# Performance work log

Hardware: AMD Instinct MI355X
Metric: run time of the kernel (lower is better)

The kernel has to match this reference:

```python
import jax, jax.numpy as jnp
import numpy as np

B, D_IN, D_H, D_BOT, D_EXP, N_CLS = 8192, 1024, 2048, 512, 1024, 10


def _w(key, shape):
    return jax.random.normal(key, shape, dtype=jnp.float32) * 0.02


def setup_inputs() -> dict:
    key = jax.random.key(0)
    ks = jax.random.split(key, 16)
    return {
        "x": jax.random.normal(ks[0], (B, D_IN), dtype=jnp.float32),
        "labels": jax.random.randint(ks[1], (B,), 0, N_CLS, dtype=jnp.int32),
        # encoder: 1024 -> 2048 -> 512 (ReLU after each)
        "W1": _w(ks[2], (D_IN, D_H)), "b1": jnp.zeros((D_H,), jnp.float32),
        "W2": _w(ks[3], (D_H, D_BOT)), "b2": jnp.zeros((D_BOT,), jnp.float32),
        # per-class expert MLPs (identical shapes, stacked): 512 -> 1024 -> 512, ReLU after each
        "EW1": _w(ks[4], (N_CLS, D_BOT, D_EXP)), "Eb1": jnp.zeros((N_CLS, D_EXP), jnp.float32),
        "EW2": _w(ks[5], (N_CLS, D_EXP, D_BOT)), "Eb2": jnp.zeros((N_CLS, D_BOT), jnp.float32),
        # decoder: 512 -> 2048 (ReLU) -> 1024 (no final activation)
        "DW1": _w(ks[6], (D_BOT, D_H)), "Db1": jnp.zeros((D_H,), jnp.float32),
        "DW2": _w(ks[7], (D_H, D_IN)), "Db2": jnp.zeros((D_IN,), jnp.float32),
    }


def reference(x, labels, W1, b1, W2, b2, EW1, Eb1, EW2, Eb2, DW1, Db1, DW2, Db2):
    # encoder
    h = jax.nn.relu(x @ W1 + b1)           # [B, 2048]
    h = jax.nn.relu(h @ W2 + b2)           # [B, 512]
    # class-routed experts: compute all experts densely, then gather by label
    he = jax.nn.relu(jnp.einsum('bi,eio->beo', h, EW1) + Eb1[None])   # [B, E, 1024]
    he = jax.nn.relu(jnp.einsum('beh,eho->beo', he, EW2) + Eb2[None]) # [B, E, 512]
    sel = jnp.take_along_axis(he, labels[:, None, None].astype(jnp.int32), axis=1)[:, 0]  # [B, 512]
    # decoder (activation after first layer only)
    d = jax.nn.relu(sel @ DW1 + Db1)       # [B, 2048]
    out = d @ DW2 + Db2                    # [B, 1024]
    return out
```

## Files before the change

kernel.cpp:

```cpp
#include <hip/hip_runtime.h>
#include <hip/hip_bf16.h>
#include <stdint.h>

typedef __attribute__((ext_vector_type(8))) short bf16x8;
typedef __attribute__((ext_vector_type(4))) float f32x4;

__device__ __forceinline__ unsigned short f2bf(float f) {
  unsigned int u = __float_as_uint(f);
  u += 0x7fff + ((u >> 16) & 1);
  return (unsigned short)(u >> 16);
}

__device__ __forceinline__ void gload16(const void* g, void* l) {
  __builtin_amdgcn_global_load_lds(
      (const __attribute__((address_space(1))) void*)g,
      (__attribute__((address_space(3))) void*)l, 16, 0, 0);
}

#define Bsz   8192
#define D_IN  1024
#define D_H   2048
#define D_BOT 512
#define D_EXP 1024
#define N_CLS 10

__global__ __launch_bounds__(1024) void k_route(const int* __restrict__ lab,
                                                int* __restrict__ counts,
                                                int* __restrict__ starts,
                                                int* __restrict__ perm) {
  __shared__ int scnt[N_CLS], scur[N_CLS];
  const int t = threadIdx.x;
  if (t < N_CLS) scnt[t] = 0;
  __syncthreads();
  int myl[8];
#pragma unroll
  for (int i = 0; i < 8; ++i) {
    myl[i] = lab[t * 8 + i];
    atomicAdd(&scnt[myl[i]], 1);
  }
  __syncthreads();
  if (t == 0) {
    int s = 0;
    for (int e = 0; e < N_CLS; ++e) {
      starts[e] = s; scur[e] = s; counts[e] = scnt[e]; s += scnt[e];
    }
  }
  __syncthreads();
#pragma unroll
  for (int i = 0; i < 8; ++i) {
    int p = atomicAdd(&scur[myl[i]], 1);
    perm[p] = t * 8 + i;
  }
}

__global__ void k_cvt(const float* __restrict__ in, unsigned short* __restrict__ out) {
  int i = (blockIdx.x * blockDim.x + threadIdx.x) * 8;
  const float4* p = (const float4*)(in + i);
  float4 a = p[0], b = p[1];
  uint4 o;
  o.x = (unsigned)f2bf(a.x) | ((unsigned)f2bf(a.y) << 16);
  o.y = (unsigned)f2bf(a.z) | ((unsigned)f2bf(a.w) << 16);
  o.z = (unsigned)f2bf(b.x) | ((unsigned)f2bf(b.y) << 16);
  o.w = (unsigned)f2bf(b.z) | ((unsigned)f2bf(b.w) << 16);
  *(uint4*)(out + i) = o;
}

__global__ void k_transpose_cvt(const float* __restrict__ in, unsigned short* __restrict__ out,
                                int K, int N) {
  __shared__ float tile[32][33];
  size_t eoff = (size_t)blockIdx.z * K * N;
  in  += eoff;
  out += eoff;
  int n0 = blockIdx.x * 32, k0 = blockIdx.y * 32;
  int tx = threadIdx.x, ty = threadIdx.y;
#pragma unroll
  for (int i = 0; i < 4; i++) {
    int k = ty + i * 8;
    tile[k][tx] = in[(size_t)(k0 + k) * N + n0 + tx];
  }
  __syncthreads();
#pragma unroll
  for (int i = 0; i < 4; i++) {
    int n = ty + i * 8;
    out[(size_t)(n0 + n) * K + k0 + tx] = f2bf(tile[tx][n]);
  }
}

template <int BM, int BN, bool RELU, bool BF16OUT>
__global__ __launch_bounds__(512, 2) void k_gemm8(
    const unsigned short* __restrict__ A,
    const unsigned short* __restrict__ WT,
    const float* __restrict__ bias,
    void* __restrict__ Cv,
    int M, int N, int K) {
  constexpr int WROWS = BM / 2;
  constexpr int QR = WROWS / 2;
  constexpr int FMq = QR / 16;
  constexpr int ACH = BM / 64;
  constexpr int BCH = BN / 64;

  const int nby = gridDim.y;
  const int nwg = gridDim.x * nby;
  int orig = blockIdx.x + gridDim.x * blockIdx.y;
  int q = nwg >> 3, r = nwg & 7;
  int xcd = orig & 7, idx = orig >> 3;
  int wg = (xcd < r ? xcd * (q + 1) : r * (q + 1) + (xcd - r) * q) + idx;
  int bx = wg / nby, by = wg % nby;
  const int m0 = bx * BM, n0 = by * BN;

  __shared__ __align__(16) unsigned short As[2][BM * 64];
  __shared__ __align__(16) unsigned short Bs[2][BN * 64];

  const int t = threadIdx.x;
  const int l = t & 63;
  const int w = t >> 6;
  const int wm = w >> 2, wn = w & 3;

  const int rl = t >> 3;
  const int sl16 = (t & 7) ^ (rl & 7);
  const unsigned short* asrc[ACH];
  const unsigned short* bsrc[BCH];
#pragma unroll
  for (int i = 0; i < ACH; ++i)
    asrc[i] = A + (size_t)(m0 + i * 64 + rl) * K + sl16 * 8;
#pragma unroll
  for (int i = 0; i < BCH; ++i)
    bsrc[i] = WT + (size_t)(n0 + i * 64 + rl) * K + sl16 * 8;
  const int dst = t * 8;

  auto STAGE = [&](int kt, int buf) {
#pragma unroll
    for (int i = 0; i < ACH; ++i)
      gload16(asrc[i] + kt * 64, &As[buf][i * 4096 + dst]);
#pragma unroll
    for (int i = 0; i < BCH; ++i)
      gload16(bsrc[i] + kt * 64, &Bs[buf][i * 4096 + dst]);
  };

  f32x4 acc[2][2][FMq][2] = {};
  bf16x8 af[FMq][2];
  bf16x8 bq[2][2][2];

  const int la = l & 15;
  const int ko = l >> 4;
  const int arow0 = wm * WROWS + la;
  const int brow0 = wn * 64 + la;

  const int nt = K / 64;
  STAGE(0, 0);

  for (int kt = 0; kt < nt; ++kt) {
    const int cur = kt & 1;
    const char* Ab = (const char*)As[cur];
    const char* Bb = (const char*)Bs[cur];

    asm volatile("s_waitcnt vmcnt(0)" ::: "memory");
    __builtin_amdgcn_s_barrier();
    if (kt + 1 < nt) STAGE(kt + 1, cur ^ 1);
    __builtin_amdgcn_sched_barrier(0);

#pragma unroll
    for (int fm = 0; fm < FMq; ++fm)
#pragma unroll
      for (int ks = 0; ks < 2; ++ks) {
        int row = arow0 + fm * 16;
        int s = ks * 4 + ko;
        af[fm][ks] = *(const bf16x8*)(Ab + (row << 7) + ((s ^ (row & 7)) << 4));
      }
#pragma unroll
    for (int fn = 0; fn < 2; ++fn)
#pragma unroll
      for (int ks = 0; ks < 2; ++ks) {
        int row = brow0 + fn * 16;
        int s = ks * 4 + ko;
        bq[0][fn][ks] = *(const bf16x8*)(Bb + (row << 7) + ((s ^ (row & 7)) << 4));
      }
    __builtin_amdgcn_s_setprio(1);
#pragma unroll
    for (int fm = 0; fm < FMq; ++fm)
#pragma unroll
      for (int fn = 0; fn < 2; ++fn)
#pragma unroll
        for (int ks = 0; ks < 2; ++ks)
          acc[0][0][fm][fn] = __builtin_amdgcn_mfma_f32_16x16x32_bf16(
              af[fm][ks], bq[0][fn][ks], acc[0][0][fm][fn], 0, 0, 0);
    __builtin_amdgcn_s_setprio(0);
    __builtin_amdgcn_s_barrier();

#pragma unroll
    for (int fn = 0; fn < 2; ++fn)
#pragma unroll
      for (int ks = 0; ks < 2; ++ks) {
        int row = brow0 + 32 + fn * 16;
        int s = ks * 4 + ko;
        bq[1][fn][ks] = *(const bf16x8*)(Bb + (row << 7) + ((s ^ (row & 7)) << 4));
      }
    __builtin_amdgcn_s_setprio(1);
#pragma unroll
    for (int fm = 0; fm < FMq; ++fm)
#pragma unroll
      for (int fn = 0; fn < 2; ++fn)
#pragma unroll
        for (int ks = 0; ks < 2; ++ks)
          acc[0][1][fm][fn] = __builtin_amdgcn_mfma_f32_16x16x32_bf16(
              af[fm][ks], bq[1][fn][ks], acc[0][1][fm][fn], 0, 0, 0);
    __builtin_amdgcn_s_setprio(0);
    __builtin_amdgcn_s_barrier();

#pragma unroll
    for (int fm = 0; fm < FMq; ++fm)
#pragma unroll
      for (int ks = 0; ks < 2; ++ks) {
        int row = arow0 + QR + fm * 16;
        int s = ks * 4 + ko;
        af[fm][ks] = *(const bf16x8*)(Ab + (row << 7) + ((s ^ (row & 7)) << 4));
      }
    __builtin_amdgcn_s_setprio(1);
#pragma unroll
    for (int fm = 0; fm < FMq; ++fm)
#pragma unroll
      for (int fn = 0; fn < 2; ++fn)
#pragma unroll
        for (int ks = 0; ks < 2; ++ks)
          acc[1][0][fm][fn] = __builtin_amdgcn_mfma_f32_16x16x32_bf16(
              af[fm][ks], bq[0][fn][ks], acc[1][0][fm][fn], 0, 0, 0);
    __builtin_amdgcn_s_setprio(0);
    __builtin_amdgcn_s_barrier();

    __builtin_amdgcn_s_setprio(1);
#pragma unroll
    for (int fm = 0; fm < FMq; ++fm)
#pragma unroll
      for (int fn = 0; fn < 2; ++fn)
#pragma unroll
        for (int ks = 0; ks < 2; ++ks)
          acc[1][1][fm][fn] = __builtin_amdgcn_mfma_f32_16x16x32_bf16(
              af[fm][ks], bq[1][fn][ks], acc[1][1][fm][fn], 0, 0, 0);
    __builtin_amdgcn_s_setprio(0);
  }
  asm volatile("s_waitcnt vmcnt(0)" ::: "memory");

  const int crow0 = m0 + wm * WROWS;
  const int ccol0 = n0 + wn * 64;
#pragma unroll
  for (int qn = 0; qn < 2; ++qn)
#pragma unroll
    for (int fn = 0; fn < 2; ++fn) {
      int c = ccol0 + qn * 32 + fn * 16 + la;
      float bv = bias[c];
#pragma unroll
      for (int qm = 0; qm < 2; ++qm)
#pragma unroll
        for (int fm = 0; fm < FMq; ++fm)
#pragma unroll
          for (int j = 0; j < 4; ++j) {
            int rr = crow0 + qm * QR + fm * 16 + (ko << 2) + j;
            float v = acc[qm][qn][fm][fn][j] + bv;
            if (RELU) v = fmaxf(v, 0.0f);
            if (BF16OUT) ((unsigned short*)Cv)[(size_t)rr * N + c] = f2bf(v);
            else         ((float*)Cv)[(size_t)rr * N + c] = v;
          }
    }
}

template <int TBM, int TBN, int WM, int WN,
          bool RELU, bool BF16OUT, bool GROUPED, bool SCATTER, bool GATHER>
__global__ __launch_bounds__(256) void k_gemm(
    const unsigned short* __restrict__ A,
    const unsigned short* __restrict__ WT,
    const float* __restrict__ bias,
    void* __restrict__ Cv,
    int M, int N, int K,
    const int* __restrict__ starts, const int* __restrict__ counts,
    const int* __restrict__ perm) {
  constexpr int FM = TBM / WM / 16;
  constexpr int FN = TBN / WN / 16;
  constexpr int ALOADS = TBM / 64;
  constexpr int BLOADS = TBN / 64;
  constexpr int LDS_LD = ALOADS + BLOADS;

  const int nby = gridDim.y;
  const int nwg = gridDim.x * nby;
  int orig = blockIdx.x + gridDim.x * blockIdx.y;
  int q = nwg >> 3, r = nwg & 7;
  int xcd = orig & 7, idx = orig >> 3;
  int wg = (xcd < r ? xcd * (q + 1) : r * (q + 1) + (xcd - r) * q) + idx;
  int bx = wg / nby, by = wg % nby;

  int Meff, start = 0, mo;
  const unsigned short* Wp = WT;
  const float* biasp = bias;
  if (GROUPED) {
    int bxr = bx;
    int found = 0;
#pragma unroll
    for (int e = 0; e < N_CLS; ++e) {
      int c = counts[e];
      int nb = (c + TBM - 1) / TBM;
      if (!found && bxr < nb) {
        found = 1; Meff = c; start = starts[e]; mo = bxr * TBM;
        Wp = WT + (size_t)e * N * K; biasp = bias + (size_t)e * N;
      }
      if (!found) bxr -= nb;
    }
    if (!found) return;
    if (!GATHER) A += (size_t)start * K;
  } else {
    Meff = M; mo = bx * TBM;
  }
  const int n0 = by * TBN;

  __shared__ __align__(16) unsigned short As[3][TBM * 32];
  __shared__ __align__(16) unsigned short Bs[3][TBN * 32];

  const int t = threadIdx.x;
  const int l = t & 63;
  const int w = t >> 6;
  const int wm = (w / WN) * (TBM / WM);
  const int wn = (w % WN) * (TBN / WN);

  const int srow = t >> 2;
  const int scol = (t & 3) * 8;
  const unsigned short* ag[ALOADS];
  const unsigned short* bg[BLOADS];
#pragma unroll
  for (int i = 0; i < ALOADS; ++i) {
    int arow = mo + srow + i * 64;
    if (GROUPED) arow = arow < Meff ? arow : Meff - 1;
    int srcrow = GATHER ? perm[start + arow] : arow;
    ag[i] = A + (size_t)srcrow * K + scol;
  }
#pragma unroll
  for (int i = 0; i < BLOADS; ++i)
    bg[i] = Wp + (size_t)(n0 + srow + i * 64) * K + scol;

  auto STAGE = [&](int buf) {
#pragma unroll
    for (int i = 0; i < ALOADS; ++i) {
      gload16(ag[i], &As[buf][t * 8 + i * 2048]);
      ag[i] += 32;
    }
#pragma unroll
    for (int i = 0; i < BLOADS; ++i) {
      gload16(bg[i], &Bs[buf][t * 8 + i * 2048]);
      bg[i] += 32;
    }
  };

  f32x4 acc[FM][FN] = {};

  const int nt = K / 32;
  STAGE(0);
  STAGE(1);
  for (int tI = 0; tI < nt; ++tI) {
    if (tI + 1 < nt)
      asm volatile("s_waitcnt vmcnt(%0)" :: "i"(LDS_LD) : "memory");
    else
      asm volatile("s_waitcnt vmcnt(0)" ::: "memory");
    __builtin_amdgcn_s_barrier();
    __builtin_amdgcn_sched_barrier(0);
    if (tI + 2 < nt) STAGE((tI + 2) % 3);

    const int cur = tI % 3;
    bf16x8 af[FM], bfr[FN];
#pragma unroll
    for (int i = 0; i < FM; ++i)
      af[i] = *(const bf16x8*)(&As[cur][(wm + i * 16 + (l & 15)) * 32 + (l >> 4) * 8]);
#pragma unroll
    for (int i = 0; i < FN; ++i)
      bfr[i] = *(const bf16x8*)(&Bs[cur][(wn + i * 16 + (l & 15)) * 32 + (l >> 4) * 8]);
#pragma unroll
    for (int mi = 0; mi < FM; ++mi)
#pragma unroll
      for (int ni = 0; ni < FN; ++ni)
        acc[mi][ni] = __builtin_amdgcn_mfma_f32_16x16x32_bf16(af[mi], bfr[ni], acc[mi][ni], 0, 0, 0);
  }

  const int cb = n0 + wn + (l & 15);
#pragma unroll
  for (int ni = 0; ni < FN; ++ni) {
    int c = cb + ni * 16;
    float bv = biasp[c];
#pragma unroll
    for (int mi = 0; mi < FM; ++mi) {
#pragma unroll
      for (int j = 0; j < 4; ++j) {
        int rl2 = wm + mi * 16 + ((l >> 4) << 2) + j;
        int re = mo + rl2;
        if (GROUPED && re >= Meff) continue;
        float v = acc[mi][ni][j] + bv;
        if (RELU) v = fmaxf(v, 0.0f);
        int orow;
        if (SCATTER)      orow = perm[start + re];
        else if (GROUPED) orow = start + re;
        else              orow = re;
        if (BF16OUT) ((unsigned short*)Cv)[(size_t)orow * N + c] = f2bf(v);
        else         ((float*)Cv)[(size_t)orow * N + c] = v;
      }
    }
  }
}

#define GX_GROUPED 74

extern "C" void kernel_launch(void* const* d_in, const int* in_sizes, int n_in,
                              void* d_out, int out_size, void* d_ws, size_t ws_size,
                              hipStream_t stream) {
  const float* x      = (const float*)d_in[0];
  const int*   labels = (const int*)d_in[1];
  const float* W1  = (const float*)d_in[2];  const float* b1  = (const float*)d_in[3];
  const float* W2  = (const float*)d_in[4];  const float* b2  = (const float*)d_in[5];
  const float* EW1 = (const float*)d_in[6];  const float* Eb1 = (const float*)d_in[7];
  const float* EW2 = (const float*)d_in[8];  const float* Eb2 = (const float*)d_in[9];
  const float* DW1 = (const float*)d_in[10]; const float* Db1 = (const float*)d_in[11];
  const float* DW2 = (const float*)d_in[12]; const float* Db2 = (const float*)d_in[13];
  float* out = (float*)d_out;

  char* ws = (char*)d_ws;
  size_t o = 0;
  unsigned short* W1T  = (unsigned short*)(ws + o); o += (size_t)D_IN * D_H * 2;
  unsigned short* W2T  = (unsigned short*)(ws + o); o += (size_t)D_H * D_BOT * 2;
  unsigned short* EW1T = (unsigned short*)(ws + o); o += (size_t)N_CLS * D_BOT * D_EXP * 2;
  unsigned short* EW2T = (unsigned short*)(ws + o); o += (size_t)N_CLS * D_EXP * D_BOT * 2;
  unsigned short* DW1T = (unsigned short*)(ws + o); o += (size_t)D_BOT * D_H * 2;
  unsigned short* DW2T = (unsigned short*)(ws + o); o += (size_t)D_H * D_IN * 2;
  unsigned short* xb   = (unsigned short*)(ws + o); o += (size_t)Bsz * D_IN * 2;
  unsigned short* e1p  = xb;
  unsigned short* actA = (unsigned short*)(ws + o); o += (size_t)Bsz * D_H * 2;
  unsigned short* h2   = (unsigned short*)(ws + o); o += (size_t)Bsz * D_BOT * 2;
  unsigned short* sel  = (unsigned short*)(ws + o); o += (size_t)Bsz * D_BOT * 2;
  int* counts = (int*)(ws + o);
  int* starts = counts + 16;
  int* perm   = counts + 64;

  k_route<<<1, 1024, 0, stream>>>(labels, counts, starts, perm);

  k_cvt<<<(Bsz * D_IN) / (256 * 8), 256, 0, stream>>>(x, xb);
  k_transpose_cvt<<<dim3(D_H / 32, D_IN / 32, 1),  dim3(32, 8), 0, stream>>>(W1, W1T, D_IN, D_H);
  k_transpose_cvt<<<dim3(D_BOT / 32, D_H / 32, 1), dim3(32, 8), 0, stream>>>(W2, W2T, D_H, D_BOT);
  k_transpose_cvt<<<dim3(D_EXP / 32, D_BOT / 32, N_CLS), dim3(32, 8), 0, stream>>>(EW1, EW1T, D_BOT, D_EXP);
  k_transpose_cvt<<<dim3(D_BOT / 32, D_EXP / 32, N_CLS), dim3(32, 8), 0, stream>>>(EW2, EW2T, D_EXP, D_BOT);
  k_transpose_cvt<<<dim3(D_H / 32, D_BOT / 32, 1), dim3(32, 8), 0, stream>>>(DW1, DW1T, D_BOT, D_H);
  k_transpose_cvt<<<dim3(D_IN / 32, D_H / 32, 1),  dim3(32, 8), 0, stream>>>(DW2, DW2T, D_H, D_IN);

  k_gemm8<256, 256, true, true><<<dim3(Bsz / 256, D_H / 256), 512, 0, stream>>>(
      xb, W1T, b1, actA, Bsz, D_H, D_IN);
  k_gemm<128, 64, 4, 1, true, true, false, false, false><<<dim3(Bsz / 128, D_BOT / 64), 256, 0, stream>>>(
      actA, W2T, b2, h2, Bsz, D_BOT, D_H, nullptr, nullptr, nullptr);

  k_gemm<128, 128, 2, 2, true, true, true, false, true><<<dim3(GX_GROUPED, D_EXP / 128), 256, 0, stream>>>(
      h2, EW1T, Eb1, e1p, Bsz, D_EXP, D_BOT, starts, counts, perm);
  k_gemm<128, 64, 4, 1, true, true, true, true, false><<<dim3(GX_GROUPED, D_BOT / 64), 256, 0, stream>>>(
      e1p, EW2T, Eb2, sel, Bsz, D_BOT, D_EXP, starts, counts, perm);

  k_gemm8<256, 256, true, true><<<dim3(Bsz / 256, D_H / 256), 512, 0, stream>>>(
      sel, DW1T, Db1, actA, Bsz, D_H, D_BOT);
  k_gemm8<128, 256, false, false><<<dim3(Bsz / 128, D_IN / 256), 512, 0, stream>>>(
      actA, DW2T, Db2, out, Bsz, D_IN, D_H);
}
```

Before: 252.5 us.

## Triple-buffer gemm8 LDS with staggered prefetch and fix tile to 128x256

The 8-wave GEMM kernel now uses three LDS buffers instead of two and keeps two k-tiles in flight. Global-to-LDS loads for tile kt+2 are split into three groups interleaved between the MFMA phases, and a partial vmcnt wait replaces the full drain at the top of each iteration. The tile is hard-coded to 128x256, so the two GEMMs that used 256x256 tiles now launch twice as many workgroups with less reuse per block. The kernel uses 144KB of LDS and adds extra barriers per iteration, which can limit occupancy to one block per CU.

```diff
diff --git a/kernel.cpp b/kernel.cpp
--- a/kernel.cpp
+++ b/kernel.cpp
@@ -86,18 +86,14 @@
   }
 }
 
-template <int BM, int BN, bool RELU, bool BF16OUT>
+template <bool RELU, bool BF16OUT>
 __global__ __launch_bounds__(512, 2) void k_gemm8(
     const unsigned short* __restrict__ A,
     const unsigned short* __restrict__ WT,
     const float* __restrict__ bias,
     void* __restrict__ Cv,
     int M, int N, int K) {
-  constexpr int WROWS = BM / 2;
-  constexpr int QR = WROWS / 2;
-  constexpr int FMq = QR / 16;
-  constexpr int ACH = BM / 64;
-  constexpr int BCH = BN / 64;
+  constexpr int BM = 128, BN = 256;
 
   const int nby = gridDim.y;
   const int nwg = gridDim.x * nby;
@@ -108,8 +104,8 @@
   int bx = wg / nby, by = wg % nby;
   const int m0 = bx * BM, n0 = by * BN;
 
-  __shared__ __align__(16) unsigned short As[2][BM * 64];
-  __shared__ __align__(16) unsigned short Bs[2][BN * 64];
+  __shared__ __align__(16) unsigned short As[3][BM * 64];
+  __shared__ __align__(16) unsigned short Bs[3][BN * 64];
 
   const int t = threadIdx.x;
   const int l = t & 63;
@@ -118,49 +114,52 @@
 
   const int rl = t >> 3;
   const int sl16 = (t & 7) ^ (rl & 7);
-  const unsigned short* asrc[ACH];
-  const unsigned short* bsrc[BCH];
-#pragma unroll
-  for (int i = 0; i < ACH; ++i)
+  const unsigned short* asrc[2];
+  const unsigned short* bsrc[4];
+#pragma unroll
+  for (int i = 0; i < 2; ++i)
     asrc[i] = A + (size_t)(m0 + i * 64 + rl) * K + sl16 * 8;
 #pragma unroll
-  for (int i = 0; i < BCH; ++i)
+  for (int i = 0; i < 4; ++i)
     bsrc[i] = WT + (size_t)(n0 + i * 64 + rl) * K + sl16 * 8;
   const int dst = t * 8;
 
-  auto STAGE = [&](int kt, int buf) {
-#pragma unroll
-    for (int i = 0; i < ACH; ++i)
-      gload16(asrc[i] + kt * 64, &As[buf][i * 4096 + dst]);
-#pragma unroll
-    for (int i = 0; i < BCH; ++i)
-      gload16(bsrc[i] + kt * 64, &Bs[buf][i * 4096 + dst]);
-  };
-
-  f32x4 acc[2][2][FMq][2] = {};
-  bf16x8 af[FMq][2];
+  f32x4 acc[2][2][2][2] = {};
+  bf16x8 af[2][2];
   bf16x8 bq[2][2][2];
 
   const int la = l & 15;
   const int ko = l >> 4;
-  const int arow0 = wm * WROWS + la;
+  const int arow0 = wm * 64 + la;
   const int brow0 = wn * 64 + la;
 
   const int nt = K / 64;
-  STAGE(0, 0);
+#pragma unroll
+  for (int i = 0; i < 2; ++i) gload16(asrc[i], &As[0][i * 4096 + dst]);
+#pragma unroll
+  for (int i = 0; i < 4; ++i) gload16(bsrc[i], &Bs[0][i * 4096 + dst]);
+#pragma unroll
+  for (int i = 0; i < 2; ++i) gload16(asrc[i] + 64, &As[1][i * 4096 + dst]);
+#pragma unroll
+  for (int i = 0; i < 4; ++i) gload16(bsrc[i] + 64, &Bs[1][i * 4096 + dst]);
 
   for (int kt = 0; kt < nt; ++kt) {
-    const int cur = kt & 1;
+    const int cur = kt % 3;
+    const int pre = (kt + 2) % 3;
+    const bool more = (kt + 2) < nt;
+    const int kk = (kt + 2) * 64;
     const char* Ab = (const char*)As[cur];
     const char* Bb = (const char*)Bs[cur];
 
-    asm volatile("s_waitcnt vmcnt(0)" ::: "memory");
-    __builtin_amdgcn_s_barrier();
-    if (kt + 1 < nt) STAGE(kt + 1, cur ^ 1);
+    if (kt + 1 < nt)
+      asm volatile("s_waitcnt vmcnt(6)" ::: "memory");
+    else
+      asm volatile("s_waitcnt vmcnt(0)" ::: "memory");
+    __builtin_amdgcn_s_barrier();
     __builtin_amdgcn_sched_barrier(0);
 
 #pragma unroll
-    for (int fm = 0; fm < FMq; ++fm)
+    for (int fm = 0; fm < 2; ++fm)
 #pragma unroll
       for (int ks = 0; ks < 2; ++ks) {
         int row = arow0 + fm * 16;
@@ -175,9 +174,15 @@
         int s = ks * 4 + ko;
         bq[0][fn][ks] = *(const bf16x8*)(Bb + (row << 7) + ((s ^ (row & 7)) << 4));
       }
+    if (more) {
+      gload16(asrc[0] + kk, &As[pre][0 * 4096 + dst]);
+      gload16(asrc[1] + kk, &As[pre][1 * 4096 + dst]);
+    }
+    __builtin_amdgcn_sched_barrier(0);
+    __builtin_amdgcn_s_barrier();
     __builtin_amdgcn_s_setprio(1);
 #pragma unroll
-    for (int fm = 0; fm < FMq; ++fm)
+    for (int fm = 0; fm < 2; ++fm)
 #pragma unroll
       for (int fn = 0; fn < 2; ++fn)
 #pragma unroll
@@ -195,9 +200,15 @@
         int s = ks * 4 + ko;
         bq[1][fn][ks] = *(const bf16x8*)(Bb + (row << 7) + ((s ^ (row & 7)) << 4));
       }
+    if (more) {
+      gload16(bsrc[0] + kk, &Bs[pre][0 * 4096 + dst]);
+      gload16(bsrc[1] + kk, &Bs[pre][1 * 4096 + dst]);
+    }
+    __builtin_amdgcn_sched_barrier(0);
+    __builtin_amdgcn_s_barrier();
     __builtin_amdgcn_s_setprio(1);
 #pragma unroll
-    for (int fm = 0; fm < FMq; ++fm)
+    for (int fm = 0; fm < 2; ++fm)
 #pragma unroll
       for (int fn = 0; fn < 2; ++fn)
 #pragma unroll
@@ -208,16 +219,22 @@
     __builtin_amdgcn_s_barrier();
 
 #pragma unroll
-    for (int fm = 0; fm < FMq; ++fm)
+    for (int fm = 0; fm < 2; ++fm)
 #pragma unroll
       for (int ks = 0; ks < 2; ++ks) {
-        int row = arow0 + QR + fm * 16;
+        int row = arow0 + 32 + fm * 16;
         int s = ks * 4 + ko;
         af[fm][ks] = *(const bf16x8*)(Ab + (row << 7) + ((s ^ (row & 7)) << 4));
       }
+    if (more) {
+      gload16(bsrc[2] + kk, &Bs[pre][2 * 4096 + dst]);
+      gload16(bsrc[3] + kk, &Bs[pre][3 * 4096 + dst]);
+    }
+    __builtin_amdgcn_sched_barrier(0);
+    __builtin_amdgcn_s_barrier();
     __builtin_amdgcn_s_setprio(1);
 #pragma unroll
-    for (int fm = 0; fm < FMq; ++fm)
+    for (int fm = 0; fm < 2; ++fm)
 #pragma unroll
       for (int fn = 0; fn < 2; ++fn)
 #pragma unroll
@@ -229,7 +246,7 @@
 
     __builtin_amdgcn_s_setprio(1);
 #pragma unroll
-    for (int fm = 0; fm < FMq; ++fm)
+    for (int fm = 0; fm < 2; ++fm)
 #pragma unroll
       for (int fn = 0; fn < 2; ++fn)
 #pragma unroll
@@ -238,9 +255,8 @@
               af[fm][ks], bq[1][fn][ks], acc[1][1][fm][fn], 0, 0, 0);
     __builtin_amdgcn_s_setprio(0);
   }
-  asm volatile("s_waitcnt vmcnt(0)" ::: "memory");
-
-  const int crow0 = m0 + wm * WROWS;
+
+  const int crow0 = m0 + wm * 64;
   const int ccol0 = n0 + wn * 64;
 #pragma unroll
   for (int qn = 0; qn < 2; ++qn)
@@ -251,10 +267,10 @@
 #pragma unroll
       for (int qm = 0; qm < 2; ++qm)
 #pragma unroll
-        for (int fm = 0; fm < FMq; ++fm)
+        for (int fm = 0; fm < 2; ++fm)
 #pragma unroll
           for (int j = 0; j < 4; ++j) {
-            int rr = crow0 + qm * QR + fm * 16 + (ko << 2) + j;
+            int rr = crow0 + qm * 32 + fm * 16 + (ko << 2) + j;
             float v = acc[qm][qn][fm][fn][j] + bv;
             if (RELU) v = fmaxf(v, 0.0f);
             if (BF16OUT) ((unsigned short*)Cv)[(size_t)rr * N + c] = f2bf(v);
@@ -443,7 +459,7 @@
   k_transpose_cvt<<<dim3(D_H / 32, D_BOT / 32, 1), dim3(32, 8), 0, stream>>>(DW1, DW1T, D_BOT, D_H);
   k_transpose_cvt<<<dim3(D_IN / 32, D_H / 32, 1),  dim3(32, 8), 0, stream>>>(DW2, DW2T, D_H, D_IN);
 
-  k_gemm8<256, 256, true, true><<<dim3(Bsz / 256, D_H / 256), 512, 0, stream>>>(
+  k_gemm8<true, true><<<dim3(Bsz / 128, D_H / 256), 512, 0, stream>>>(
       xb, W1T, b1, actA, Bsz, D_H, D_IN);
   k_gemm<128, 64, 4, 1, true, true, false, false, false><<<dim3(Bsz / 128, D_BOT / 64), 256, 0, stream>>>(
       actA, W2T, b2, h2, Bsz, D_BOT, D_H, nullptr, nullptr, nullptr);
@@ -453,8 +469,8 @@
   k_gemm<128, 64, 4, 1, true, true, true, true, false><<<dim3(GX_GROUPED, D_BOT / 64), 256, 0, stream>>>(
       e1p, EW2T, Eb2, sel, Bsz, D_BOT, D_EXP, starts, counts, perm);
 
-  k_gemm8<256, 256, true, true><<<dim3(Bsz / 256, D_H / 256), 512, 0, stream>>>(
+  k_gemm8<true, true><<<dim3(Bsz / 128, D_H / 256), 512, 0, stream>>>(
       sel, DW1T, Db1, actA, Bsz, D_H, D_BOT);
-  k_gemm8<128, 256, false, false><<<dim3(Bsz / 128, D_IN / 256), 512, 0, stream>>>(
+  k_gemm8<false, false><<<dim3(Bsz / 128, D_IN / 256), 512, 0, stream>>>(
       actA, DW2T, Db2, out, Bsz, D_IN, D_H);
 }
```

Measured after the change: 255.2 us. Within noise of the previous version (+1.1%).

## Simplify gemm8 to fixed 256x256 tile with per-row-fragment MFMA loop

Applied to the files above, without the earlier changes.

Rewrites the 8-wave GEMM inner loop to load all four B fragments once per k-step, then stream the eight A row fragments one at a time with MFMAs. This drops the quadrant-phased schedule and its intra-iteration barriers. The template is specialised to a fixed 256x256 tile, so the last decoder GEMM now uses 256-row tiles, and the W2 encoder GEMM tile grows from 128 to 256 rows. The cost is fewer workgroups on those GEMMs and possibly less overlap of LDS reads with MFMA work.

```diff
diff --git a/kernel.cpp b/kernel.cpp
--- a/kernel.cpp
+++ b/kernel.cpp
@@ -86,18 +86,14 @@
   }
 }
 
-template <int BM, int BN, bool RELU, bool BF16OUT>
+template <bool RELU, bool BF16OUT>
 __global__ __launch_bounds__(512, 2) void k_gemm8(
     const unsigned short* __restrict__ A,
     const unsigned short* __restrict__ WT,
     const float* __restrict__ bias,
     void* __restrict__ Cv,
     int M, int N, int K) {
-  constexpr int WROWS = BM / 2;
-  constexpr int QR = WROWS / 2;
-  constexpr int FMq = QR / 16;
-  constexpr int ACH = BM / 64;
-  constexpr int BCH = BN / 64;
+  constexpr int BM = 256, BN = 256;
 
   const int nby = gridDim.y;
   const int nwg = gridDim.x * nby;
@@ -118,32 +114,31 @@
 
   const int rl = t >> 3;
   const int sl16 = (t & 7) ^ (rl & 7);
-  const unsigned short* asrc[ACH];
-  const unsigned short* bsrc[BCH];
-#pragma unroll
-  for (int i = 0; i < ACH; ++i)
+  const unsigned short* asrc[4];
+  const unsigned short* bsrc[4];
+#pragma unroll
+  for (int i = 0; i < 4; ++i) {
     asrc[i] = A + (size_t)(m0 + i * 64 + rl) * K + sl16 * 8;
-#pragma unroll
-  for (int i = 0; i < BCH; ++i)
     bsrc[i] = WT + (size_t)(n0 + i * 64 + rl) * K + sl16 * 8;
+  }
   const int dst = t * 8;
 
   auto STAGE = [&](int kt, int buf) {
 #pragma unroll
-    for (int i = 0; i < ACH; ++i)
+    for (int i = 0; i < 4; ++i)
       gload16(asrc[i] + kt * 64, &As[buf][i * 4096 + dst]);
 #pragma unroll
-    for (int i = 0; i < BCH; ++i)
+    for (int i = 0; i < 4; ++i)
       gload16(bsrc[i] + kt * 64, &Bs[buf][i * 4096 + dst]);
   };
 
-  f32x4 acc[2][2][FMq][2] = {};
-  bf16x8 af[FMq][2];
-  bf16x8 bq[2][2][2];
+  f32x4 acc[8][4] = {};
+  bf16x8 bq[4][2];
+  bf16x8 af[2];
 
   const int la = l & 15;
   const int ko = l >> 4;
-  const int arow0 = wm * WROWS + la;
+  const int arow0 = wm * 128 + la;
   const int brow0 = wn * 64 + la;
 
   const int nt = K / 64;
@@ -160,107 +155,50 @@
     __builtin_amdgcn_sched_barrier(0);
 
 #pragma unroll
-    for (int fm = 0; fm < FMq; ++fm)
-#pragma unroll
-      for (int ks = 0; ks < 2; ++ks) {
-        int row = arow0 + fm * 16;
-        int s = ks * 4 + ko;
-        af[fm][ks] = *(const bf16x8*)(Ab + (row << 7) + ((s ^ (row & 7)) << 4));
-      }
-#pragma unroll
-    for (int fn = 0; fn < 2; ++fn)
+    for (int fn = 0; fn < 4; ++fn)
 #pragma unroll
       for (int ks = 0; ks < 2; ++ks) {
         int row = brow0 + fn * 16;
         int s = ks * 4 + ko;
-        bq[0][fn][ks] = *(const bf16x8*)(Bb + (row << 7) + ((s ^ (row & 7)) << 4));
-      }
-    __builtin_amdgcn_s_setprio(1);
-#pragma unroll
-    for (int fm = 0; fm < FMq; ++fm)
-#pragma unroll
-      for (int fn = 0; fn < 2; ++fn)
+        bq[fn][ks] = *(const bf16x8*)(Bb + (row << 7) + ((s ^ (row & 7)) << 4));
+      }
+
+#pragma unroll
+    for (int fm = 0; fm < 8; ++fm) {
+      int row = arow0 + fm * 16;
+#pragma unroll
+      for (int ks = 0; ks < 2; ++ks) {
+        int s = ks * 4 + ko;
+        af[ks] = *(const bf16x8*)(Ab + (row << 7) + ((s ^ (row & 7)) << 4));
+      }
+      __builtin_amdgcn_s_setprio(1);
+#pragma unroll
+      for (int fn = 0; fn < 4; ++fn)
 #pragma unroll
         for (int ks = 0; ks < 2; ++ks)
-          acc[0][0][fm][fn] = __builtin_amdgcn_mfma_f32_16x16x32_bf16(
-              af[fm][ks], bq[0][fn][ks], acc[0][0][fm][fn], 0, 0, 0);
-    __builtin_amdgcn_s_setprio(0);
-    __builtin_amdgcn_s_barrier();
-
-#pragma unroll
-    for (int fn = 0; fn < 2; ++fn)
-#pragma unroll
-      for (int ks = 0; ks < 2; ++ks) {
-        int row = brow0 + 32 + fn * 16;
-        int s = ks * 4 + ko;
-        bq[1][fn][ks] = *(const bf16x8*)(Bb + (row << 7) + ((s ^ (row & 7)) << 4));
-      }
-    __builtin_amdgcn_s_setprio(1);
-#pragma unroll
-    for (int fm = 0; fm < FMq; ++fm)
-#pragma unroll
-      for (int fn = 0; fn < 2; ++fn)
-#pragma unroll
-        for (int ks = 0; ks < 2; ++ks)
-          acc[0][1][fm][fn] = __builtin_amdgcn_mfma_f32_16x16x32_bf16(
-              af[fm][ks], bq[1][fn][ks], acc[0][1][fm][fn], 0, 0, 0);
-    __builtin_amdgcn_s_setprio(0);
-    __builtin_amdgcn_s_barrier();
-
-#pragma unroll
-    for (int fm = 0; fm < FMq; ++fm)
-#pragma unroll
-      for (int ks = 0; ks < 2; ++ks) {
-        int row = arow0 + QR + fm * 16;
-        int s = ks * 4 + ko;
-        af[fm][ks] = *(const bf16x8*)(Ab + (row << 7) + ((s ^ (row & 7)) << 4));
-      }
-    __builtin_amdgcn_s_setprio(1);
-#pragma unroll
-    for (int fm = 0; fm < FMq; ++fm)
-#pragma unroll
-      for (int fn = 0; fn < 2; ++fn)
-#pragma unroll
-        for (int ks = 0; ks < 2; ++ks)
-          acc[1][0][fm][fn] = __builtin_amdgcn_mfma_f32_16x16x32_bf16(
-              af[fm][ks], bq[0][fn][ks], acc[1][0][fm][fn], 0, 0, 0);
-    __builtin_amdgcn_s_setprio(0);
-    __builtin_amdgcn_s_barrier();
-
-    __builtin_amdgcn_s_setprio(1);
-#pragma unroll
-    for (int fm = 0; fm < FMq; ++fm)
-#pragma unroll
-      for (int fn = 0; fn < 2; ++fn)
-#pragma unroll
-        for (int ks = 0; ks < 2; ++ks)
-          acc[1][1][fm][fn] = __builtin_amdgcn_mfma_f32_16x16x32_bf16(
-              af[fm][ks], bq[1][fn][ks], acc[1][1][fm][fn], 0, 0, 0);
-    __builtin_amdgcn_s_setprio(0);
-  }
-  asm volatile("s_waitcnt vmcnt(0)" ::: "memory");
-
-  const int crow0 = m0 + wm * WROWS;
+          acc[fm][fn] = __builtin_amdgcn_mfma_f32_16x16x32_bf16(
+              af[ks], bq[fn][ks], acc[fm][fn], 0, 0, 0);
+      __builtin_amdgcn_s_setprio(0);
+    }
+  }
+
+  const int crow0 = m0 + wm * 128;
   const int ccol0 = n0 + wn * 64;
 #pragma unroll
-  for (int qn = 0; qn < 2; ++qn)
-#pragma unroll
-    for (int fn = 0; fn < 2; ++fn) {
-      int c = ccol0 + qn * 32 + fn * 16 + la;
-      float bv = bias[c];
-#pragma unroll
-      for (int qm = 0; qm < 2; ++qm)
-#pragma unroll
-        for (int fm = 0; fm < FMq; ++fm)
-#pragma unroll
-          for (int j = 0; j < 4; ++j) {
-            int rr = crow0 + qm * QR + fm * 16 + (ko << 2) + j;
-            float v = acc[qm][qn][fm][fn][j] + bv;
-            if (RELU) v = fmaxf(v, 0.0f);
-            if (BF16OUT) ((unsigned short*)Cv)[(size_t)rr * N + c] = f2bf(v);
-            else         ((float*)Cv)[(size_t)rr * N + c] = v;
-          }
-    }
+  for (int fn = 0; fn < 4; ++fn) {
+    int c = ccol0 + fn * 16 + la;
+    float bv = bias[c];
+#pragma unroll
+    for (int fm = 0; fm < 8; ++fm)
+#pragma unroll
+      for (int j = 0; j < 4; ++j) {
+        int rr = crow0 + fm * 16 + (ko << 2) + j;
+        float v = acc[fm][fn][j] + bv;
+        if (RELU) v = fmaxf(v, 0.0f);
+        if (BF16OUT) ((unsigned short*)Cv)[(size_t)rr * N + c] = f2bf(v);
+        else         ((float*)Cv)[(size_t)rr * N + c] = v;
+      }
+  }
 }
 
 template <int TBM, int TBN, int WM, int WN,
@@ -443,9 +381,9 @@
   k_transpose_cvt<<<dim3(D_H / 32, D_BOT / 32, 1), dim3(32, 8), 0, stream>>>(DW1, DW1T, D_BOT, D_H);
   k_transpose_cvt<<<dim3(D_IN / 32, D_H / 32, 1),  dim3(32, 8), 0, stream>>>(DW2, DW2T, D_H, D_IN);
 
-  k_gemm8<256, 256, true, true><<<dim3(Bsz / 256, D_H / 256), 512, 0, stream>>>(
+  k_gemm8<true, true><<<dim3(Bsz / 256, D_H / 256), 512, 0, stream>>>(
       xb, W1T, b1, actA, Bsz, D_H, D_IN);
-  k_gemm<128, 64, 4, 1, true, true, false, false, false><<<dim3(Bsz / 128, D_BOT / 64), 256, 0, stream>>>(
+  k_gemm<256, 64, 4, 1, true, true, false, false, false><<<dim3(Bsz / 256, D_BOT / 64), 256, 0, stream>>>(
       actA, W2T, b2, h2, Bsz, D_BOT, D_H, nullptr, nullptr, nullptr);
 
   k_gemm<128, 128, 2, 2, true, true, true, false, true><<<dim3(GX_GROUPED, D_EXP / 128), 256, 0, stream>>>(
@@ -453,8 +391,8 @@
   k_gemm<128, 64, 4, 1, true, true, true, true, false><<<dim3(GX_GROUPED, D_BOT / 64), 256, 0, stream>>>(
       e1p, EW2T, Eb2, sel, Bsz, D_BOT, D_EXP, starts, counts, perm);
 
-  k_gemm8<256, 256, true, true><<<dim3(Bsz / 256, D_H / 256), 512, 0, stream>>>(
+  k_gemm8<true, true><<<dim3(Bsz / 256, D_H / 256), 512, 0, stream>>>(
       sel, DW1T, Db1, actA, Bsz, D_H, D_BOT);
-  k_gemm8<128, 256, false, false><<<dim3(Bsz / 128, D_IN / 256), 512, 0, stream>>>(
+  k_gemm8<false, false><<<dim3(Bsz / 256, D_IN / 256), 512, 0, stream>>>(
       actA, DW2T, Db2, out, Bsz, D_IN, D_H);
 }
```

Measured after the change: 283.4 us. 1.12x slower.

## Fuse input fp32-to-bf16 conversion into first GEMM and merge weight transposes

Applied to the files above, without the earlier changes.

Removes the separate x conversion kernel by having the first GEMM load fp32 activations, convert them to bf16 in registers and write them to LDS. The six weight transpose/convert launches are merged into one kernel that dispatches by block index. This cuts launch overhead and one full pass over x. In exchange, A loads in the first GEMM become synchronous register loads instead of async LDS loads, and fp32 re-reads double that GEMM's A traffic.

```diff
diff --git a/kernel.cpp b/kernel.cpp
--- a/kernel.cpp
+++ b/kernel.cpp
@@ -53,42 +53,45 @@
   }
 }
 
-__global__ void k_cvt(const float* __restrict__ in, unsigned short* __restrict__ out) {
-  int i = (blockIdx.x * blockDim.x + threadIdx.x) * 8;
-  const float4* p = (const float4*)(in + i);
-  float4 a = p[0], b = p[1];
-  uint4 o;
-  o.x = (unsigned)f2bf(a.x) | ((unsigned)f2bf(a.y) << 16);
-  o.y = (unsigned)f2bf(a.z) | ((unsigned)f2bf(a.w) << 16);
-  o.z = (unsigned)f2bf(b.x) | ((unsigned)f2bf(b.y) << 16);
-  o.w = (unsigned)f2bf(b.z) | ((unsigned)f2bf(b.w) << 16);
-  *(uint4*)(out + i) = o;
-}
-
-__global__ void k_transpose_cvt(const float* __restrict__ in, unsigned short* __restrict__ out,
-                                int K, int N) {
-  __shared__ float tile[32][33];
-  size_t eoff = (size_t)blockIdx.z * K * N;
-  in  += eoff;
-  out += eoff;
-  int n0 = blockIdx.x * 32, k0 = blockIdx.y * 32;
-  int tx = threadIdx.x, ty = threadIdx.y;
-#pragma unroll
-  for (int i = 0; i < 4; i++) {
+__global__ void k_prep(const float* __restrict__ W1,  const float* __restrict__ W2,
+                       const float* __restrict__ EW1, const float* __restrict__ EW2,
+                       const float* __restrict__ DW1, const float* __restrict__ DW2,
+                       unsigned short* __restrict__ W1T,  unsigned short* __restrict__ W2T,
+                       unsigned short* __restrict__ EW1T, unsigned short* __restrict__ EW2T,
+                       unsigned short* __restrict__ DW1T, unsigned short* __restrict__ DW2T) {
+  const int bid = blockIdx.x;
+  const float* in; unsigned short* out; int K, N, tile;
+  if (bid < 2048)        { in = W1;  out = W1T;  K = D_IN;  N = D_H;   tile = bid; }
+  else if (bid < 3072)   { in = W2;  out = W2T;  K = D_H;   N = D_BOT; tile = bid - 2048; }
+  else if (bid < 8192)   { int r = bid - 3072; int e = r >> 9; tile = r & 511;
+                           K = D_BOT; N = D_EXP;
+                           in = EW1 + (size_t)e * K * N; out = EW1T + (size_t)e * K * N; }
+  else if (bid < 13312)  { int r = bid - 8192; int e = r >> 9; tile = r & 511;
+                           K = D_EXP; N = D_BOT;
+                           in = EW2 + (size_t)e * K * N; out = EW2T + (size_t)e * K * N; }
+  else if (bid < 14336)  { in = DW1; out = DW1T; K = D_BOT; N = D_H;   tile = bid - 13312; }
+  else                   { in = DW2; out = DW2T; K = D_H;   N = D_IN;  tile = bid - 14336; }
+  const int ntx = N >> 5;
+  const int n0 = (tile % ntx) * 32, k0 = (tile / ntx) * 32;
+
+  __shared__ float tl[32][33];
+  const int tx = threadIdx.x, ty = threadIdx.y;
+#pragma unroll
+  for (int i = 0; i < 4; ++i) {
     int k = ty + i * 8;
-    tile[k][tx] = in[(size_t)(k0 + k) * N + n0 + tx];
+    tl[k][tx] = in[(size_t)(k0 + k) * N + n0 + tx];
   }
   __syncthreads();
 #pragma unroll
-  for (int i = 0; i < 4; i++) {
+  for (int i = 0; i < 4; ++i) {
     int n = ty + i * 8;
-    out[(size_t)(n0 + n) * K + k0 + tx] = f2bf(tile[tx][n]);
-  }
-}
-
-template <int BM, int BN, bool RELU, bool BF16OUT>
+    out[(size_t)(n0 + n) * K + k0 + tx] = f2bf(tl[tx][n]);
+  }
+}
+
+template <int BM, int BN, bool RELU, bool BF16OUT, bool AFP32>
 __global__ __launch_bounds__(512, 2) void k_gemm8(
-    const unsigned short* __restrict__ A,
+    const void* __restrict__ Av,
     const unsigned short* __restrict__ WT,
     const float* __restrict__ bias,
     void* __restrict__ Cv,
@@ -118,20 +121,40 @@
 
   const int rl = t >> 3;
   const int sl16 = (t & 7) ^ (rl & 7);
-  const unsigned short* asrc[ACH];
+  const unsigned short* a16[ACH];
+  const float* a32[ACH];
   const unsigned short* bsrc[BCH];
 #pragma unroll
-  for (int i = 0; i < ACH; ++i)
-    asrc[i] = A + (size_t)(m0 + i * 64 + rl) * K + sl16 * 8;
+  for (int i = 0; i < ACH; ++i) {
+    if constexpr (AFP32)
+      a32[i] = (const float*)Av + (size_t)(m0 + i * 64 + rl) * K + sl16 * 8;
+    else
+      a16[i] = (const unsigned short*)Av + (size_t)(m0 + i * 64 + rl) * K + sl16 * 8;
+  }
 #pragma unroll
   for (int i = 0; i < BCH; ++i)
     bsrc[i] = WT + (size_t)(n0 + i * 64 + rl) * K + sl16 * 8;
   const int dst = t * 8;
 
   auto STAGE = [&](int kt, int buf) {
-#pragma unroll
-    for (int i = 0; i < ACH; ++i)
-      gload16(asrc[i] + kt * 64, &As[buf][i * 4096 + dst]);
+    if constexpr (AFP32) {
+#pragma unroll
+      for (int i = 0; i < ACH; ++i) {
+        const float* s = a32[i] + kt * 64;
+        float4 lo = *(const float4*)s;
+        float4 hi = *(const float4*)(s + 4);
+        uint4 o;
+        o.x = (unsigned)f2bf(lo.x) | ((unsigned)f2bf(lo.y) << 16);
+        o.y = (unsigned)f2bf(lo.z) | ((unsigned)f2bf(lo.w) << 16);
+        o.z = (unsigned)f2bf(hi.x) | ((unsigned)f2bf(hi.y) << 16);
+        o.w = (unsigned)f2bf(hi.z) | ((unsigned)f2bf(hi.w) << 16);
+        *(uint4*)(&As[buf][i * 4096 + dst]) = o;
+      }
+    } else {
+#pragma unroll
+      for (int i = 0; i < ACH; ++i)
+        gload16(a16[i] + kt * 64, &As[buf][i * 4096 + dst]);
+    }
 #pragma unroll
     for (int i = 0; i < BCH; ++i)
       gload16(bsrc[i] + kt * 64, &Bs[buf][i * 4096 + dst]);
@@ -154,7 +177,10 @@
     const char* Ab = (const char*)As[cur];
     const char* Bb = (const char*)Bs[cur];
 
-    asm volatile("s_waitcnt vmcnt(0)" ::: "memory");
+    if constexpr (AFP32)
+      asm volatile("s_waitcnt vmcnt(0) lgkmcnt(0)" ::: "memory");
+    else
+      asm volatile("s_waitcnt vmcnt(0)" ::: "memory");
     __builtin_amdgcn_s_barrier();
     if (kt + 1 < nt) STAGE(kt + 1, cur ^ 1);
     __builtin_amdgcn_sched_barrier(0);
@@ -424,8 +450,7 @@
   unsigned short* EW2T = (unsigned short*)(ws + o); o += (size_t)N_CLS * D_EXP * D_BOT * 2;
   unsigned short* DW1T = (unsigned short*)(ws + o); o += (size_t)D_BOT * D_H * 2;
   unsigned short* DW2T = (unsigned short*)(ws + o); o += (size_t)D_H * D_IN * 2;
-  unsigned short* xb   = (unsigned short*)(ws + o); o += (size_t)Bsz * D_IN * 2;
-  unsigned short* e1p  = xb;
+  unsigned short* e1p  = (unsigned short*)(ws + o); o += (size_t)Bsz * D_EXP * 2;
   unsigned short* actA = (unsigned short*)(ws + o); o += (size_t)Bsz * D_H * 2;
   unsigned short* h2   = (unsigned short*)(ws + o); o += (size_t)Bsz * D_BOT * 2;
   unsigned short* sel  = (unsigned short*)(ws + o); o += (size_t)Bsz * D_BOT * 2;
@@ -435,16 +460,11 @@
 
   k_route<<<1, 1024, 0, stream>>>(labels, counts, starts, perm);
 
-  k_cvt<<<(Bsz * D_IN) / (256 * 8), 256, 0, stream>>>(x, xb);
-  k_transpose_cvt<<<dim3(D_H / 32, D_IN / 32, 1),  dim3(32, 8), 0, stream>>>(W1, W1T, D_IN, D_H);
-  k_transpose_cvt<<<dim3(D_BOT / 32, D_H / 32, 1), dim3(32, 8), 0, stream>>>(W2, W2T, D_H, D_BOT);
-  k_transpose_cvt<<<dim3(D_EXP / 32, D_BOT / 32, N_CLS), dim3(32, 8), 0, stream>>>(EW1, EW1T, D_BOT, D_EXP);
-  k_transpose_cvt<<<dim3(D_BOT / 32, D_EXP / 32, N_CLS), dim3(32, 8), 0, stream>>>(EW2, EW2T, D_EXP, D_BOT);
-  k_transpose_cvt<<<dim3(D_H / 32, D_BOT / 32, 1), dim3(32, 8), 0, stream>>>(DW1, DW1T, D_BOT, D_H);
-  k_transpose_cvt<<<dim3(D_IN / 32, D_H / 32, 1),  dim3(32, 8), 0, stream>>>(DW2, DW2T, D_H, D_IN);
-
-  k_gemm8<256, 256, true, true><<<dim3(Bsz / 256, D_H / 256), 512, 0, stream>>>(
-      xb, W1T, b1, actA, Bsz, D_H, D_IN);
+  k_prep<<<16384, dim3(32, 8), 0, stream>>>(W1, W2, EW1, EW2, DW1, DW2,
+                                            W1T, W2T, EW1T, EW2T, DW1T, DW2T);
+
+  k_gemm8<256, 256, true, true, true><<<dim3(Bsz / 256, D_H / 256), 512, 0, stream>>>(
+      x, W1T, b1, actA, Bsz, D_H, D_IN);
   k_gemm<128, 64, 4, 1, true, true, false, false, false><<<dim3(Bsz / 128, D_BOT / 64), 256, 0, stream>>>(
       actA, W2T, b2, h2, Bsz, D_BOT, D_H, nullptr, nullptr, nullptr);
 
@@ -453,8 +473,8 @@
   k_gemm<128, 64, 4, 1, true, true, true, true, false><<<dim3(GX_GROUPED, D_BOT / 64), 256, 0, stream>>>(
       e1p, EW2T, Eb2, sel, Bsz, D_BOT, D_EXP, starts, counts, perm);
 
-  k_gemm8<256, 256, true, true><<<dim3(Bsz / 256, D_H / 256), 512, 0, stream>>>(
+  k_gemm8<256, 256, true, true, false><<<dim3(Bsz / 256, D_H / 256), 512, 0, stream>>>(
       sel, DW1T, Db1, actA, Bsz, D_H, D_BOT);
-  k_gemm8<128, 256, false, false><<<dim3(Bsz / 128, D_IN / 256), 512, 0, stream>>>(
+  k_gemm8<128, 256, false, false, false><<<dim3(Bsz / 128, D_IN / 256), 512, 0, stream>>>(
       actA, DW2T, Db2, out, Bsz, D_IN, D_H);
 }
```

Result: faster. 244.1 us (-3.3%).
